# Kernel tuning notes

Measured on AMD Instinct MI355X. Metric: run time of the kernel, lower is better.

## Reference

```python
import jax, jax.numpy as jnp
import numpy as np

N = 100000   # nodes
E = 1200000  # edges
FIN = 128    # in_channels
H = 64       # hidden_channels
OUT = 1      # out_channels


def setup_inputs() -> dict:
    key = jax.random.key(0)
    ks = jax.random.split(key, 12)
    s = 0.05
    return {
        "x": jax.random.normal(ks[0], (N, FIN), jnp.float32),
        "edge_index": jax.random.randint(ks[1], (2, E), 0, N, dtype=jnp.int64),
        "W0": jax.random.normal(ks[2], (FIN, H), jnp.float32) * s,
        "b0": jnp.zeros((H,), jnp.float32),
        "W1": jax.random.normal(ks[3], (H, H), jnp.float32) * s,
        "b1": jnp.zeros((H,), jnp.float32),
        "W2": jax.random.normal(ks[4], (H, OUT), jnp.float32) * s,
        "b2": jnp.zeros((OUT,), jnp.float32),
        "Wm1": jax.random.normal(ks[5], (OUT, H), jnp.float32) * s,
        "bm1": jnp.zeros((H,), jnp.float32),
        "Wm2": jax.random.normal(ks[6], (H, OUT), jnp.float32) * s,
        "bm2": jnp.zeros((OUT,), jnp.float32),
    }


def reference(x, edge_index, W0, b0, W1, b1, W2, b2, Wm1, bm1, Wm2, bm2):
    # GCNConv (PyG default): add self-loops, symmetric normalization D^-1/2 A D^-1/2
    loop = jnp.arange(N, dtype=edge_index.dtype)
    src = jnp.concatenate([edge_index[0], loop])  # [E+N]
    dst = jnp.concatenate([edge_index[1], loop])
    deg = jax.ops.segment_sum(jnp.ones(E + N, jnp.float32), dst, num_segments=N)
    dinv = jax.lax.rsqrt(deg)  # deg >= 1 thanks to self-loops
    norm = dinv[src] * dinv[dst]  # [E+N]

    def conv(h, W, b):
        h = h @ W  # [N, d_out]
        msg = h[src] * norm[:, None]  # gather + scale, [E+N, d_out]
        return jax.ops.segment_sum(msg, dst, num_segments=N) + b

    h = jax.nn.relu(conv(x, W0, b0))   # input layer (dropout is identity in eval)
    h = jax.nn.relu(conv(h, W1, b1))   # hidden layer
    h = conv(h, W2, b2)                # output GCN layer -> [N, OUT]
    # MLP head
    h = jax.nn.relu(h @ Wm1 + bm1) @ Wm2 + bm2
    return h
```

## Files before the change

### kernel.cpp

```cpp
#include <hip/hip_runtime.h>
#include <hip/hip_fp16.h>
#include <math.h>

#define ELL_CAP 48
#define NBUCK 391
#define BCAP 3584

typedef _Float16 half8 __attribute__((ext_vector_type(8)));
typedef float floatx4 __attribute__((ext_vector_type(4)));


__device__ __forceinline__ __half2 u2h(unsigned u) {
  __half2 h; __builtin_memcpy(&h, &u, 4); return h;
}
__device__ __forceinline__ unsigned h2u(__half2 h) {
  unsigned u; __builtin_memcpy(&u, &h, 4); return u;
}


__global__ __launch_bounds__(1024) void k_bucket(const int* __restrict__ src,
                                                 const int* __restrict__ dst,
                                                 int* __restrict__ cursors,
                                                 int* __restrict__ buckets, int E) {
  __shared__ int hist[NBUCK];
  __shared__ int base[NBUCK];
  const int tid = threadIdx.x;
  for (int i = tid; i < NBUCK; i += 1024) hist[i] = 0;
  __syncthreads();

  const long s0 = (long)blockIdx.x * E / gridDim.x;
  const long s1 = (long)(blockIdx.x + 1) * E / gridDim.x;

  for (long e = s0 + tid; e < s1; e += 1024) atomicAdd(&hist[dst[e] >> 8], 1);
  __syncthreads();

  for (int i = tid; i < NBUCK; i += 1024) {
    int c = hist[i];
    base[i] = (c > 0) ? atomicAdd(&cursors[i], c) : 0;
    hist[i] = 0;
  }
  __syncthreads();

  for (long e = s0 + tid; e < s1; e += 1024) {
    int s = src[e], d = dst[e];
    int b = d >> 8;
    int pos = base[b] + atomicAdd(&hist[b], 1);
    if (pos < BCAP) buckets[(long)b * BCAP + pos] = ((d & 255) << 24) | s;
  }
}


__global__ __launch_bounds__(256) void k_ellbuild(const int* __restrict__ buckets,
                                                  const int* __restrict__ cursors,
                                                  int* __restrict__ cnt,
                                                  int* __restrict__ ell,
                                                  float* __restrict__ dinv,
                                                  __half* __restrict__ zrow, int n) {
  __shared__ int cnt_l[256];
  __shared__ int ell_l[256 * ELL_CAP];
  const int b = blockIdx.x, tid = threadIdx.x;
  cnt_l[tid] = 0;
  if (b == 0 && tid < 64) zrow[tid] = __float2half(0.f);
  __syncthreads();

  int m = cursors[b];
  if (m > BCAP) m = BCAP;
  const int* bk = buckets + (long)b * BCAP;
  for (int i = tid; i < m; i += 256) {
    int p = bk[i];
    int ld = ((unsigned)p) >> 24;
    int pos = atomicAdd(&cnt_l[ld], 1);
    if (pos < ELL_CAP) ell_l[ld * ELL_CAP + pos] = p & 0xFFFFFF;
  }
  __syncthreads();

  const int d0 = b << 8;
  const int node = d0 + tid;
  if (node < n) {
    int c = cnt_l[tid];
    if (c > ELL_CAP) c = ELL_CAP;
    cnt[node] = c;
    dinv[node] = 1.0f / sqrtf((float)(c + 1));
  }
  const int rows = min(256, n - d0);
  const int lim4 = rows * ELL_CAP / 4;
  int4* dst4 = (int4*)(ell + (long)d0 * ELL_CAP);
  const int4* src4 = (const int4*)ell_l;
  for (int i = tid; i < lim4; i += 256) dst4[i] = src4[i];
}


template <int K, bool RELU, bool IN_HALF>
__global__ __launch_bounds__(256) void k_gemm_mfma(const void* __restrict__ Xv,
                                                   const float* __restrict__ W,
                                                   const float* __restrict__ dinv,
                                                   __half* __restrict__ out, int n) {
  constexpr int SP = K + 8;
  constexpr int NS = K / 32;
  __shared__ __half Wl[64 * SP];
  const int tx = threadIdx.x;

  for (int idx = tx; idx < (K / 2) * 64; idx += 256) {
    int k2 = idx >> 6, col = idx & 63;
    __half2 h = __floats2half2_rn(W[(2 * k2) * 64 + col], W[(2 * k2 + 1) * 64 + col]);
    *(__half2*)&Wl[col * SP + 2 * k2] = h;
  }
  __syncthreads();

  const int lane = tx & 63;
  const int l15 = lane & 15;
  const int quad = lane >> 4;
  const long base = (long)blockIdx.x * 64 + (tx >> 6) * 16;

  long arow = base + l15;
  if (arow >= n) arow = n - 1;
  const float* Xf = (const float*)Xv;
  const __half* Xh = (const __half*)Xv;

  half8 afrag[NS];
#pragma unroll
  for (int s = 0; s < NS; ++s) {
    if constexpr (IN_HALF) {
      afrag[s] = *(const half8*)&Xh[arow * K + s * 32 + quad * 8];
    } else {
      float4 lo = *(const float4*)&Xf[arow * K + s * 32 + quad * 8];
      float4 hi = *(const float4*)&Xf[arow * K + s * 32 + quad * 8 + 4];
      half8 a;
      a[0] = (_Float16)lo.x; a[1] = (_Float16)lo.y;
      a[2] = (_Float16)lo.z; a[3] = (_Float16)lo.w;
      a[4] = (_Float16)hi.x; a[5] = (_Float16)hi.y;
      a[6] = (_Float16)hi.z; a[7] = (_Float16)hi.w;
      afrag[s] = a;
    }
    if (RELU) {
      unsigned short* u = (unsigned short*)&afrag[s];
#pragma unroll
      for (int j = 0; j < 8; ++j) u[j] = (u[j] & 0x8000) ? (unsigned short)0 : u[j];
    }
  }

  floatx4 acc[4];
#pragma unroll
  for (int t = 0; t < 4; ++t) acc[t] = (floatx4){0.f, 0.f, 0.f, 0.f};

#pragma unroll
  for (int s = 0; s < NS; ++s) {
#pragma unroll
    for (int t = 0; t < 4; ++t) {
      half8 bfrag = *(const half8*)&Wl[(t * 16 + l15) * SP + s * 32 + quad * 8];
      acc[t] = __builtin_amdgcn_mfma_f32_16x16x32_f16(afrag[s], bfrag, acc[t], 0, 0, 0);
    }
  }

#pragma unroll
  for (int r = 0; r < 4; ++r) {
    long node = base + quad * 4 + r;
    if (node < n) {
      float dv = dinv[node];
#pragma unroll
      for (int t = 0; t < 4; ++t)
        out[node * 64 + t * 16 + l15] = __float2half(acc[t][r] * dv);
    }
  }
}


template <typename EPI>
__device__ __forceinline__ void gather8(const __half* __restrict__ hs,
                                        const int* __restrict__ ell,
                                        const int* __restrict__ cnt,
                                        const float* __restrict__ dinv,
                                        int n, EPI epi) {
  const int tid = threadIdx.x;
  const int lane = tid & 63;
  const int l8 = lane & 7;
  const int wave = (blockIdx.x * 256 + tid) >> 6;
  const int node = wave * 8 + (lane >> 3);
  const bool alive = node < n;
  const int nd = alive ? node : 0;
  const int c = alive ? cnt[nd] : 0;
  const float di = alive ? dinv[nd] : 0.f;
  const int* row = &ell[(long)nd * ELL_CAP];

  int s0 = (l8 < c) ? row[l8] : n;
  int s1 = (8 + l8 < c) ? row[8 + l8] : n;
  int s2 = (16 + l8 < c) ? row[16 + l8] : n;

  int cm = c;
  cm = max(cm, __shfl_xor(cm, 8, 64));
  cm = max(cm, __shfl_xor(cm, 16, 64));
  cm = max(cm, __shfl_xor(cm, 32, 64));
  const int nph = (cm + 7) >> 3;

  float accf[8];
  {
    float4 v = alive ? *(const float4*)&hs[(long)nd * 64 + l8 * 8]
                     : make_float4(0.f, 0.f, 0.f, 0.f);
    const unsigned* up = (const unsigned*)&v;
#pragma unroll
    for (int t = 0; t < 4; ++t) {
      float2 f = __half22float2(u2h(up[t]));
      accf[2 * t] = f.x; accf[2 * t + 1] = f.y;
    }
  }

  auto phase = [&](int reg) {
    int ss[8];
#pragma unroll
    for (int u = 0; u < 8; ++u) ss[u] = __shfl(reg, u, 8);
    float4 vv[8];
#pragma unroll
    for (int u = 0; u < 8; ++u) vv[u] = *(const float4*)&hs[(long)ss[u] * 64 + l8 * 8];
#pragma unroll
    for (int u = 0; u < 8; ++u) {
      const unsigned* up = (const unsigned*)&vv[u];
#pragma unroll
      for (int t = 0; t < 4; ++t) {
        float2 f = __half22float2(u2h(up[t]));
        accf[2 * t] += f.x; accf[2 * t + 1] += f.y;
      }
    }
  };

  if (nph > 0) phase(s0);
  if (nph > 1) phase(s1);
  if (nph > 2) phase(s2);
  for (int ph = 3; ph < nph; ++ph) {
    int reg = (ph * 8 + l8 < c) ? row[ph * 8 + l8] : n;
    phase(reg);
  }

  epi(accf, di, node, l8, alive);
}

__global__ __launch_bounds__(256) void k_gather64x8(const __half* __restrict__ hs,
                                                    const int* __restrict__ ell,
                                                    const int* __restrict__ cnt,
                                                    const float* __restrict__ dinv,
                                                    const float* __restrict__ b,
                                                    __half* __restrict__ agg, int n) {
  gather8(hs, ell, cnt, dinv, n,
          [&](const float (&accf)[8], float di, int node, int l8, bool alive) {
    if (!alive) return;
    float4 bv0 = *(const float4*)&b[l8 * 8];
    float4 bv1 = *(const float4*)&b[l8 * 8 + 4];
    uint4 o;
    o.x = h2u(__floats2half2_rn(bv0.x + di * accf[0], bv0.y + di * accf[1]));
    o.y = h2u(__floats2half2_rn(bv0.z + di * accf[2], bv0.w + di * accf[3]));
    o.z = h2u(__floats2half2_rn(bv1.x + di * accf[4], bv1.y + di * accf[5]));
    o.w = h2u(__floats2half2_rn(bv1.z + di * accf[6], bv1.w + di * accf[7]));
    *(uint4*)&agg[(long)node * 64 + l8 * 8] = o;
  });
}

__global__ __launch_bounds__(256) void k_gather64x8_dot(const __half* __restrict__ hs,
                                                        const int* __restrict__ ell,
                                                        const int* __restrict__ cnt,
                                                        const float* __restrict__ dinv,
                                                        const float* __restrict__ b1,
                                                        const float* __restrict__ W2,
                                                        float* __restrict__ h2, int n) {
  gather8(hs, ell, cnt, dinv, n,
          [&](const float (&accf)[8], float di, int node, int l8, bool alive) {
    float4 bv0 = *(const float4*)&b1[l8 * 8];
    float4 bv1 = *(const float4*)&b1[l8 * 8 + 4];
    float4 wv0 = *(const float4*)&W2[l8 * 8];
    float4 wv1 = *(const float4*)&W2[l8 * 8 + 4];
    float part = fmaxf(bv0.x + di * accf[0], 0.f) * wv0.x;
    part = fmaf(fmaxf(bv0.y + di * accf[1], 0.f), wv0.y, part);
    part = fmaf(fmaxf(bv0.z + di * accf[2], 0.f), wv0.z, part);
    part = fmaf(fmaxf(bv0.w + di * accf[3], 0.f), wv0.w, part);
    part = fmaf(fmaxf(bv1.x + di * accf[4], 0.f), wv1.x, part);
    part = fmaf(fmaxf(bv1.y + di * accf[5], 0.f), wv1.y, part);
    part = fmaf(fmaxf(bv1.z + di * accf[6], 0.f), wv1.z, part);
    part = fmaf(fmaxf(bv1.w + di * accf[7], 0.f), wv1.w, part);
#pragma unroll
    for (int off = 1; off < 8; off <<= 1) part += __shfl_xor(part, off, 8);
    if (alive && l8 == 0) h2[node] = part;
  });
}


__global__ void k_gather1_mlp(const float* __restrict__ h2, const int* __restrict__ ell,
                              const int* __restrict__ cnt, const float* __restrict__ dinv,
                              const float* __restrict__ b2,
                              const float* __restrict__ Wm1, const float* __restrict__ bm1,
                              const float* __restrict__ Wm2, const float* __restrict__ bm2,
                              float* __restrict__ out, int n) {
  __shared__ float w1s[64], w2s[64], b1s[64];
  if (threadIdx.x < 64) {
    w1s[threadIdx.x] = Wm1[threadIdx.x];
    w2s[threadIdx.x] = Wm2[threadIdx.x];
    b1s[threadIdx.x] = bm1[threadIdx.x];
  }
  __syncthreads();
  int i = blockIdx.x * blockDim.x + threadIdx.x;
  if (i >= n) return;
  int c = cnt[i];
  float di = dinv[i];
  float acc = di * h2[i];
  const int* row = &ell[(long)i * ELL_CAP];
  for (int j = 0; j < c; ++j) {
    int s = row[j];
    acc = fmaf(dinv[s], h2[s], acc);
  }
  float sv = b2[0] + di * acc;
  float o = bm2[0];
#pragma unroll
  for (int j = 0; j < 64; ++j)
    o = fmaf(fmaxf(fmaf(sv, w1s[j], b1s[j]), 0.f), w2s[j], o);
  out[i] = o;
}


extern "C" void kernel_launch(void* const* d_in, const int* in_sizes, int n_in,
                              void* d_out, int out_size, void* d_ws, size_t ws_size,
                              hipStream_t stream) {
  const float* x   = (const float*)d_in[0];
  const int*   ei  = (const int*)d_in[1];
  const float* W0  = (const float*)d_in[2];
  const float* b0  = (const float*)d_in[3];
  const float* W1  = (const float*)d_in[4];
  const float* b1  = (const float*)d_in[5];
  const float* W2  = (const float*)d_in[6];
  const float* b2  = (const float*)d_in[7];
  const float* Wm1 = (const float*)d_in[8];
  const float* bm1 = (const float*)d_in[9];
  const float* Wm2 = (const float*)d_in[10];
  const float* bm2 = (const float*)d_in[11];

  const int n = in_sizes[0] / 128;
  const int E = in_sizes[1] / 2;
  const int* src = ei;
  const int* dst = ei + E;

  float*  ws   = (float*)d_ws;
  float*  dinv = ws;
  int*    cnt  = (int*)(ws + n);
  int*    ell  = cnt + n;
  __half* bufA = (__half*)(ell + (size_t)n * ELL_CAP);
  __half* bufB = bufA + (size_t)(n + 1) * 64;
  float*  h2   = (float*)(bufB + (size_t)n * 64);
  int*    cursors = (int*)(h2 + n);
  int*    buckets = (int*)bufA;

  const int nb  = (n + 255) / 256;
  const int g8b = (((n + 7) / 8) + 3) / 4;
  const int mfb = (n + 63) / 64;

  hipMemsetAsync(cursors, 0, NBUCK * sizeof(int), stream);
  k_bucket<<<256, 1024, 0, stream>>>(src, dst, cursors, buckets, E);
  k_ellbuild<<<NBUCK, 256, 0, stream>>>(buckets, cursors, cnt, ell, dinv,
                                        bufA + (size_t)n * 64, n);

  k_gemm_mfma<128, false, false><<<mfb, 256, 0, stream>>>(x, W0, dinv, bufA, n);
  k_gather64x8<<<g8b, 256, 0, stream>>>(bufA, ell, cnt, dinv, b0, bufB, n);

  k_gemm_mfma<64, true, true><<<mfb, 256, 0, stream>>>(bufB, W1, dinv, bufA, n);
  k_gather64x8_dot<<<g8b, 256, 0, stream>>>(bufA, ell, cnt, dinv, b1, W2, h2, n);

  k_gather1_mlp<<<nb, 256, 0, stream>>>(h2, ell, cnt, dinv, b2, Wm1, bm1, Wm2, bm2,
                                        (float*)d_out, n);
}
```

Baseline: 223.3 us.

## Degree-sort nodes per bucket and parallelize final scalar gather across lanes

Builds a per-bucket remap that orders nodes by in-degree so each wave's 8 node groups have similar neighbor counts, reducing divergence in the gather loops. The final scalar aggregation moves from one thread per node to 8 lanes per node with a shuffle reduction, with h2 prescaled by dinv so the gather avoids per-neighbor dinv loads. The MLP head becomes a separate kernel. This adds a remap indirection, an extra launch, and writes scattered by remapped node order.

New measurement: 234.2 us. 1.05x slower.

```diff
diff --git a/kernel.cpp b/kernel.cpp
--- a/kernel.cpp
+++ b/kernel.cpp
@@ -55,11 +55,15 @@
                                                   int* __restrict__ cnt,
                                                   int* __restrict__ ell,
                                                   float* __restrict__ dinv,
+                                                  int* __restrict__ remap,
                                                   __half* __restrict__ zrow, int n) {
   __shared__ int cnt_l[256];
   __shared__ int ell_l[256 * ELL_CAP];
+  __shared__ int dh[64];
+  __shared__ int dbase[64];
   const int b = blockIdx.x, tid = threadIdx.x;
   cnt_l[tid] = 0;
+  if (tid < 64) dh[tid] = 0;
   if (b == 0 && tid < 64) zrow[tid] = __float2half(0.f);
   __syncthreads();
 
@@ -76,13 +80,26 @@
 
   const int d0 = b << 8;
   const int node = d0 + tid;
-  if (node < n) {
-    int c = cnt_l[tid];
+  const int rows = min(256, n - d0);
+  int c = 0;
+  if (tid < rows) {
+    c = cnt_l[tid];
     if (c > ELL_CAP) c = ELL_CAP;
     cnt[node] = c;
     dinv[node] = 1.0f / sqrtf((float)(c + 1));
-  }
-  const int rows = min(256, n - d0);
+    atomicAdd(&dh[c], 1);
+  }
+  __syncthreads();
+  if (tid == 0) {
+    int s = 0;
+    for (int i = 0; i < 64; ++i) { dbase[i] = s; s += dh[i]; }
+  }
+  __syncthreads();
+  if (tid < rows) {
+    int r = atomicAdd(&dbase[c], 1);
+    remap[d0 + r] = node;
+  }
+
   const int lim4 = rows * ELL_CAP / 4;
   int4* dst4 = (int4*)(ell + (long)d0 * ELL_CAP);
   const int4* src4 = (const int4*)ell_l;
@@ -170,21 +187,21 @@
                                         const int* __restrict__ ell,
                                         const int* __restrict__ cnt,
                                         const float* __restrict__ dinv,
+                                        const int* __restrict__ remap,
                                         int n, EPI epi) {
   const int tid = threadIdx.x;
   const int lane = tid & 63;
   const int l8 = lane & 7;
   const int wave = (blockIdx.x * 256 + tid) >> 6;
-  const int node = wave * 8 + (lane >> 3);
-  const bool alive = node < n;
-  const int nd = alive ? node : 0;
+  const int slot = wave * 8 + (lane >> 3);
+  const bool alive = slot < n;
+  const int nd = alive ? remap[slot] : 0;
   const int c = alive ? cnt[nd] : 0;
   const float di = alive ? dinv[nd] : 0.f;
   const int* row = &ell[(long)nd * ELL_CAP];
 
   int s0 = (l8 < c) ? row[l8] : n;
   int s1 = (8 + l8 < c) ? row[8 + l8] : n;
-  int s2 = (16 + l8 < c) ? row[16 + l8] : n;
 
   int cm = c;
   cm = max(cm, __shfl_xor(cm, 8, 64));
@@ -224,22 +241,22 @@
 
   if (nph > 0) phase(s0);
   if (nph > 1) phase(s1);
-  if (nph > 2) phase(s2);
-  for (int ph = 3; ph < nph; ++ph) {
+  for (int ph = 2; ph < nph; ++ph) {
     int reg = (ph * 8 + l8 < c) ? row[ph * 8 + l8] : n;
     phase(reg);
   }
 
-  epi(accf, di, node, l8, alive);
+  epi(accf, di, nd, l8, alive);
 }
 
 __global__ __launch_bounds__(256) void k_gather64x8(const __half* __restrict__ hs,
                                                     const int* __restrict__ ell,
                                                     const int* __restrict__ cnt,
                                                     const float* __restrict__ dinv,
+                                                    const int* __restrict__ remap,
                                                     const float* __restrict__ b,
                                                     __half* __restrict__ agg, int n) {
-  gather8(hs, ell, cnt, dinv, n,
+  gather8(hs, ell, cnt, dinv, remap, n,
           [&](const float (&accf)[8], float di, int node, int l8, bool alive) {
     if (!alive) return;
     float4 bv0 = *(const float4*)&b[l8 * 8];
@@ -257,10 +274,12 @@
                                                         const int* __restrict__ ell,
                                                         const int* __restrict__ cnt,
                                                         const float* __restrict__ dinv,
+                                                        const int* __restrict__ remap,
                                                         const float* __restrict__ b1,
                                                         const float* __restrict__ W2,
-                                                        float* __restrict__ h2, int n) {
-  gather8(hs, ell, cnt, dinv, n,
+                                                        float* __restrict__ h2s, int n) {
+  if (blockIdx.x == 0 && threadIdx.x == 0) h2s[n] = 0.f;
+  gather8(hs, ell, cnt, dinv, remap, n,
           [&](const float (&accf)[8], float di, int node, int l8, bool alive) {
     float4 bv0 = *(const float4*)&b1[l8 * 8];
     float4 bv1 = *(const float4*)&b1[l8 * 8 + 4];
@@ -276,17 +295,51 @@
     part = fmaf(fmaxf(bv1.w + di * accf[7], 0.f), wv1.w, part);
 #pragma unroll
     for (int off = 1; off < 8; off <<= 1) part += __shfl_xor(part, off, 8);
-    if (alive && l8 == 0) h2[node] = part;
+    if (alive && l8 == 0) h2s[node] = di * part;
   });
 }
 
 
-__global__ void k_gather1_mlp(const float* __restrict__ h2, const int* __restrict__ ell,
-                              const int* __restrict__ cnt, const float* __restrict__ dinv,
-                              const float* __restrict__ b2,
-                              const float* __restrict__ Wm1, const float* __restrict__ bm1,
-                              const float* __restrict__ Wm2, const float* __restrict__ bm2,
-                              float* __restrict__ out, int n) {
+__global__ __launch_bounds__(256) void k_gather1x8(const float* __restrict__ h2s,
+                                                   const int* __restrict__ ell,
+                                                   const int* __restrict__ cnt,
+                                                   const float* __restrict__ dinv,
+                                                   const int* __restrict__ remap,
+                                                   const float* __restrict__ b2,
+                                                   float* __restrict__ agg2, int n) {
+  const int tid = threadIdx.x;
+  const int lane = tid & 63;
+  const int l8 = lane & 7;
+  const int wave = (blockIdx.x * 256 + tid) >> 6;
+  const int slot = wave * 8 + (lane >> 3);
+  const bool alive = slot < n;
+  const int nd = alive ? remap[slot] : 0;
+  const int c = alive ? cnt[nd] : 0;
+  const float di = alive ? dinv[nd] : 0.f;
+  const int* row = &ell[(long)nd * ELL_CAP];
+
+  int cm = c;
+  cm = max(cm, __shfl_xor(cm, 8, 64));
+  cm = max(cm, __shfl_xor(cm, 16, 64));
+  cm = max(cm, __shfl_xor(cm, 32, 64));
+  const int nph = (cm + 7) >> 3;
+
+  float acc = (alive && l8 == 0) ? h2s[nd] : 0.f;
+  for (int ph = 0; ph < nph; ++ph) {
+    int j = ph * 8 + l8;
+    int s = (j < c) ? row[j] : n;
+    acc += h2s[s];
+  }
+#pragma unroll
+  for (int off = 1; off < 8; off <<= 1) acc += __shfl_xor(acc, off, 8);
+  if (alive && l8 == 0) agg2[nd] = b2[0] + di * acc;
+}
+
+
+__global__ void k_mlp(const float* __restrict__ agg2,
+                      const float* __restrict__ Wm1, const float* __restrict__ bm1,
+                      const float* __restrict__ Wm2, const float* __restrict__ bm2,
+                      float* __restrict__ out, int n) {
   __shared__ float w1s[64], w2s[64], b1s[64];
   if (threadIdx.x < 64) {
     w1s[threadIdx.x] = Wm1[threadIdx.x];
@@ -296,19 +349,11 @@
   __syncthreads();
   int i = blockIdx.x * blockDim.x + threadIdx.x;
   if (i >= n) return;
-  int c = cnt[i];
-  float di = dinv[i];
-  float acc = di * h2[i];
-  const int* row = &ell[(long)i * ELL_CAP];
-  for (int j = 0; j < c; ++j) {
-    int s = row[j];
-    acc = fmaf(dinv[s], h2[s], acc);
-  }
-  float sv = b2[0] + di * acc;
+  float s = agg2[i];
   float o = bm2[0];
 #pragma unroll
   for (int j = 0; j < 64; ++j)
-    o = fmaf(fmaxf(fmaf(sv, w1s[j], b1s[j]), 0.f), w2s[j], o);
+    o = fmaf(fmaxf(fmaf(s, w1s[j], b1s[j]), 0.f), w2s[j], o);
   out[i] = o;
 }
 
@@ -340,8 +385,10 @@
   int*    ell  = cnt + n;
   __half* bufA = (__half*)(ell + (size_t)n * ELL_CAP);
   __half* bufB = bufA + (size_t)(n + 1) * 64;
-  float*  h2   = (float*)(bufB + (size_t)n * 64);
-  int*    cursors = (int*)(h2 + n);
+  float*  h2s  = (float*)(bufB + (size_t)n * 64);
+  float*  agg2 = h2s + (n + 1);
+  int*    remap = (int*)(agg2 + n);
+  int*    cursors = (int*)(remap + n);
   int*    buckets = (int*)bufA;
 
   const int nb  = (n + 255) / 256;
@@ -350,15 +397,15 @@
 
   hipMemsetAsync(cursors, 0, NBUCK * sizeof(int), stream);
   k_bucket<<<256, 1024, 0, stream>>>(src, dst, cursors, buckets, E);
-  k_ellbuild<<<NBUCK, 256, 0, stream>>>(buckets, cursors, cnt, ell, dinv,
+  k_ellbuild<<<NBUCK, 256, 0, stream>>>(buckets, cursors, cnt, ell, dinv, remap,
                                         bufA + (size_t)n * 64, n);
 
   k_gemm_mfma<128, false, false><<<mfb, 256, 0, stream>>>(x, W0, dinv, bufA, n);
-  k_gather64x8<<<g8b, 256, 0, stream>>>(bufA, ell, cnt, dinv, b0, bufB, n);
+  k_gather64x8<<<g8b, 256, 0, stream>>>(bufA, ell, cnt, dinv, remap, b0, bufB, n);
 
   k_gemm_mfma<64, true, true><<<mfb, 256, 0, stream>>>(bufB, W1, dinv, bufA, n);
-  k_gather64x8_dot<<<g8b, 256, 0, stream>>>(bufA, ell, cnt, dinv, b1, W2, h2, n);
-
-  k_gather1_mlp<<<nb, 256, 0, stream>>>(h2, ell, cnt, dinv, b2, Wm1, bm1, Wm2, bm2,
-                                        (float*)d_out, n);
-}
+  k_gather64x8_dot<<<g8b, 256, 0, stream>>>(bufA, ell, cnt, dinv, remap, b1, W2, h2s, n);
+
+  k_gather1x8<<<g8b, 256, 0, stream>>>(h2s, ell, cnt, dinv, remap, b2, agg2, n);
+  k_mlp<<<nb, 256, 0, stream>>>(agg2, Wm1, bm1, Wm2, bm2, (float*)d_out, n);
+}
```
